# Kernel tuning notes

Measured on AMD Instinct MI355X. Metric: run time of the kernel, lower is better.

Reference implementation:

```python
import jax, jax.numpy as jnp
import numpy as np

CODE_DIM = 512
NUM_CODEBOOKS = 4
CODEBOOK_SIZE = 1024
SUB_DIM = CODE_DIM // NUM_CODEBOOKS


def setup_inputs() -> dict:
    key = jax.random.key(0)
    k1, k2 = jax.random.split(key)
    z_e = jax.random.normal(k1, (64, 512, CODE_DIM), dtype=jnp.float32)
    bound = 1.0 / CODEBOOK_SIZE
    codebooks = jax.random.uniform(
        k2, (NUM_CODEBOOKS, CODEBOOK_SIZE, SUB_DIM),
        minval=-bound, maxval=bound, dtype=jnp.float32)
    return {"z_e": z_e, "codebooks": codebooks}


def reference(z_e, codebooks):
    B, L, D = z_e.shape
    K, S, d = codebooks.shape  # K codebooks, S entries, sub_dim d
    N = B * L
    flat = z_e.reshape(N, K, d)  # per-codebook sub-vectors
    # squared euclidean distances: [N, K, S]
    dist = ((flat ** 2).sum(-1)[:, :, None]
            - 2.0 * jnp.einsum('nkd,ksd->nks', flat, codebooks)
            + (codebooks ** 2).sum(-1)[None, :, :])
    idx = jnp.argmin(dist, axis=-1)  # [N, K]
    # gather nearest codes per codebook
    z_q = codebooks[jnp.arange(K)[None, :], idx]  # [N, K, d]
    z_q_all = z_q.reshape(B, L, D)
    # sum_k mse_k / K == mean over the full concatenated tensor
    codebook_loss = jnp.mean((z_q_all - jax.lax.stop_gradient(z_e)) ** 2)
    commit_loss = jnp.mean((z_e - jax.lax.stop_gradient(z_q_all)) ** 2)
    # perplexity via index counts (no NxS one-hot materialization)
    counts = jnp.zeros((K, S), dtype=z_e.dtype).at[
        jnp.broadcast_to(jnp.arange(K)[None, :], idx.shape), idx].add(1.0)
    avg_probs = counts / N  # [K, S]
    perplexity = jnp.exp(
        -(avg_probs * jnp.log(jnp.clip(avg_probs, 1e-8))).sum(-1)).mean()
    z_q_st = z_e + jax.lax.stop_gradient(z_q_all - z_e)
    indices_all = idx.reshape(B, L, K)
    return indices_all, z_q_st, z_q_all, codebook_loss, commit_loss, perplexity
```

## Files before the change

kernel.cpp:

```cpp
#include <hip/hip_runtime.h>
#include <math.h>

#define NVEC  32768
#define DDIM  512
#define KCB   4
#define SCB   1024
#define SUBD  128

#define IDX_COUNT (NVEC * KCB)
#define ZQ_COUNT  (NVEC * DDIM)
#define OFF_ZQ_ST  IDX_COUNT
#define OFF_ZQ_ALL (IDX_COUNT + ZQ_COUNT)
#define OFF_SCAL   (IDX_COUNT + 2 * ZQ_COUNT)


typedef _Float16 v2h __attribute__((ext_vector_type(2)));
typedef _Float16 f16x8 __attribute__((ext_vector_type(8)));
typedef float f32x16 __attribute__((ext_vector_type(16)));
union U32H2 { unsigned int u; v2h h; };

__device__ __forceinline__ float fmul(float a, float b) { return __fmul_rn(a, b); }
__device__ __forceinline__ float fadd(float a, float b) { return __fadd_rn(a, b); }
__device__ __forceinline__ float fsub(float a, float b) { return __fsub_rn(a, b); }

__device__ __forceinline__ float np_dot128(const float* __restrict__ u,
                                           const float* __restrict__ v) {
  float r[8];
#pragma unroll
  for (int j = 0; j < 8; ++j) r[j] = fmul(u[j], v[j]);
#pragma unroll
  for (int i = 8; i < 128; i += 8) {
#pragma unroll
    for (int j = 0; j < 8; ++j) r[j] = fadd(r[j], fmul(u[i + j], v[i + j]));
  }
  return fadd(fadd(fadd(r[0], r[1]), fadd(r[2], r[3])),
              fadd(fadd(r[4], r[5]), fadd(r[6], r[7])));
}

__device__ __forceinline__ int imin(int a, int b) { return a < b ? a : b; }
__device__ __forceinline__ int imax(int a, int b) { return a > b ? a : b; }

__device__ __forceinline__ void ins4(int& k0, int& k1, int& k2, int& k3, int x) {
  int a = imax(k0, x); k0 = imin(k0, x);
  int b = imax(k1, a); k1 = imin(k1, a);
  int c = imax(k2, b); k2 = imin(k2, b);
  k3 = imin(k3, c);
}

__global__ __launch_bounds__(256) void k_prep(
    const float* __restrict__ cb, unsigned int* __restrict__ cb16,
    float* __restrict__ c2s, float* __restrict__ c2np,
    int* __restrict__ counts, float* __restrict__ scal,
    int* __restrict__ ctrs) {
  const int gt = blockIdx.x * 256 + threadIdx.x;
  if (gt < KCB * SCB) counts[gt] = 0;
  if (gt < 3) scal[gt] = 0.0f;
  if (gt < 2) ctrs[gt] = 0;
  if (gt < KCB * SCB) {
    const float* row = cb + (size_t)gt * SUBD;
    c2np[gt] = np_dot128(row, row);
  }
  const int wave = blockIdx.x * 4 + (threadIdx.x >> 6);
  const int lane = threadIdx.x & 63;
  for (int i = 0; i < 16; ++i) {
    const int code = wave * 16 + i;
    const float2 v = ((const float2*)(cb + (size_t)code * SUBD))[lane];
    float tot = fmaf(v.x, v.x, v.y * v.y);
#pragma unroll
    for (int off = 32; off > 0; off >>= 1) tot += __shfl_down(tot, off, 64);
    v2h h; h.x = (_Float16)(v.x * 1024.0f); h.y = (_Float16)(v.y * 1024.0f);
    U32H2 t; t.h = h;
    cb16[(size_t)code * 64 + lane] = t.u;
    if (lane == 0) c2s[code] = tot * 1048576.0f;
  }
}

#define SCORE(ACC, STOFF, K0, K1, K2, K3)                                    \
  {                                                                          \
    _Pragma("unroll")                                                        \
    for (int g = 0; g < 4; ++g) {                                            \
      const float4 cv = *(const float4*)(c2b + (STOFF) + hi * 4 + g * 8);    \
      const float ca[4] = {cv.x, cv.y, cv.z, cv.w};                          \
      _Pragma("unroll")                                                      \
      for (int r = 0; r < 4; ++r) {                                          \
        const float sc = fmaf(-2048.0f, (ACC)[g * 4 + r], ca[r]);            \
        const int key = ((int)sc << 10) | (tb + (STOFF) + hi * 4 + g * 8 + r); \
        ins4(K0, K1, K2, K3, key);                                           \
      }                                                                      \
    }                                                                        \
  }

__device__ __forceinline__ void stage_tile(const uint4* __restrict__ gsrc,
                                           unsigned int* lds_u32,
                                           int w, int rbase, int ss) {
#pragma unroll
  for (int p = 0; p < 4; ++p) {
    const uint4* src = gsrc + (size_t)((p * 16 + rbase) * 16 + ss);
    unsigned int* dst = lds_u32 + (p * 256 + w * 64) * 4;
    __builtin_amdgcn_global_load_lds(
        (const __attribute__((address_space(1))) unsigned int*)src,
        (__attribute__((address_space(3))) unsigned int*)dst, 16, 0, 0);
  }
}

__global__ __launch_bounds__(256) void k_scan(
    const float* __restrict__ z_e, const unsigned int* __restrict__ cb16,
    const float* __restrict__ c2s, unsigned short* __restrict__ cand) {
  const int tid = threadIdx.x;
  const int lane = tid & 63;
  const int w = tid >> 6;
  const int hi = lane >> 5;
  const int ml = lane & 31;
  const int k = blockIdx.y;
  const int n = blockIdx.x * 128 + w * 32 + ml;

  __shared__ __align__(16) unsigned int ctile[2][4096];

  const uint4* gk = (const uint4*)cb16 + (size_t)k * SCB * 16;
  const float* c2k = c2s + k * SCB;
  const int rbase = tid >> 4;
  const int ss = (tid & 15) ^ rbase;

  f16x8 xf[8];
  {
    const float* xp = z_e + (size_t)n * DDIM + k * SUBD + hi * 8;
#pragma unroll
    for (int ks = 0; ks < 8; ++ks) {
      const float4 a = *(const float4*)(xp + ks * 16);
      const float4 b = *(const float4*)(xp + ks * 16 + 4);
      f16x8 h;
      h[0] = (_Float16)a.x; h[1] = (_Float16)a.y;
      h[2] = (_Float16)a.z; h[3] = (_Float16)a.w;
      h[4] = (_Float16)b.x; h[5] = (_Float16)b.y;
      h[6] = (_Float16)b.z; h[7] = (_Float16)b.w;
      xf[ks] = h;
    }
  }

  stage_tile(gk, ctile[0], w, rbase, ss);
  __syncthreads();

  int kA0 = 0x7FFFFFFF, kA1 = 0x7FFFFFFF, kA2 = 0x7FFFFFFF, kA3 = 0x7FFFFFFF;
  int kB0 = 0x7FFFFFFF, kB1 = 0x7FFFFFFF, kB2 = 0x7FFFFFFF, kB3 = 0x7FFFFFFF;

  for (int tile = 0; tile < 16; ++tile) {
    if (tile < 15)
      stage_tile(gk + (size_t)(tile + 1) * 1024, ctile[(tile + 1) & 1],
                 w, rbase, ss);

    const unsigned char* bufb = (const unsigned char*)ctile[tile & 1];
    f32x16 acc0, acc1;
#pragma unroll
    for (int z = 0; z < 16; ++z) { acc0[z] = 0.0f; acc1[z] = 0.0f; }

#pragma unroll
    for (int ks = 0; ks < 8; ++ks) {
      const int phys = (((ks * 2 + hi) ^ (lane & 15)) << 4);
      const f16x8 a0 = *(const f16x8*)(bufb + ml * 256 + phys);
      const f16x8 a1 = *(const f16x8*)(bufb + (ml + 32) * 256 + phys);
      acc0 = __builtin_amdgcn_mfma_f32_32x32x16_f16(a0, xf[ks], acc0, 0, 0, 0);
      acc1 = __builtin_amdgcn_mfma_f32_32x32x16_f16(a1, xf[ks], acc1, 0, 0, 0);
    }

    const int tb = tile * 64;
    const float* c2b = c2k + tb;
    SCORE(acc0, 0, kA0, kA1, kA2, kA3)
    SCORE(acc1, 32, kB0, kB1, kB2, kB3)

    __syncthreads();
  }

  ins4(kA0, kA1, kA2, kA3, kB0);
  ins4(kA0, kA1, kA2, kA3, kB1);
  ins4(kA0, kA1, kA2, kA3, kB2);
  ins4(kA0, kA1, kA2, kA3, kB3);

  const unsigned long long pk =
      (unsigned long long)(unsigned short)(kA0 & 1023) |
      ((unsigned long long)(unsigned short)(kA1 & 1023) << 16) |
      ((unsigned long long)(unsigned short)(kA2 & 1023) << 32) |
      ((unsigned long long)(unsigned short)(kA3 & 1023) << 48);
  *(unsigned long long*)(cand + ((size_t)(n * KCB + k)) * 8 + hi * 4) = pk;
}

__global__ __launch_bounds__(256) void k_merge(
    const float* __restrict__ z_e, const float* __restrict__ cb,
    const unsigned short* __restrict__ cand, const float* __restrict__ c2np,
    float* __restrict__ out_idx, int* __restrict__ counts,
    float* __restrict__ scal, int* __restrict__ ctrs) {
  const int tid = threadIdx.x;
  const int g = blockIdx.x * 256 + tid;
  const int n = g >> 2, k = g & 3;
  const int w = tid >> 6, lane = tid & 63;

  float4 xv[32];
  const float4* xp = (const float4*)(z_e + (size_t)n * DDIM + k * SUBD);
#pragma unroll
  for (int j = 0; j < 32; ++j) xv[j] = xp[j];
  const float* xs = (const float*)xv;
  const float A = np_dot128(xs, xs);

  const unsigned short* cp = cand + (size_t)g * 8;
  float bd = 1e30f;
  int bi = SCB;
#pragma unroll
  for (int t = 0; t < 8; ++t) {
    const int s = cp[t];
    const float* c = cb + (size_t)(k * SCB + s) * SUBD;
    const float E = np_dot128(xs, c);
    const float dist = fadd(fsub(A, fmul(2.0f, E)), c2np[k * SCB + s]);
    if (dist < bd || (dist == bd && s < bi)) { bd = dist; bi = s; }
  }

  out_idx[g] = (float)bi;
  atomicAdd(&counts[k * SCB + bi], 1);

  float local = bd;
#pragma unroll
  for (int off = 32; off > 0; off >>= 1) local += __shfl_down(local, off, 64);
  __shared__ float red[4];
  if (lane == 0) red[w] = local;
  __syncthreads();

  __shared__ int lastf;
  if (tid == 0) {
    atomicAdd(&scal[0], (red[0] + red[1]) + (red[2] + red[3]));
    __threadfence();
    lastf = (atomicAdd(&ctrs[0], 1) == (int)gridDim.x - 1);
  }
  __syncthreads();

  if (lastf) {
    double h = 0.0;
    for (int i = 0; i < SCB / 64; ++i) {
      const int cnt = __hip_atomic_load(&counts[w * SCB + i * 64 + lane],
                                        __ATOMIC_RELAXED, __HIP_MEMORY_SCOPE_AGENT);
      if (cnt > 0) {
        const double p = (double)cnt * (1.0 / 32768.0);
        h += p * log(p);
      }
    }
#pragma unroll
    for (int off = 32; off > 0; off >>= 1) h += __shfl_down(h, off, 64);
    __shared__ double hs[4];
    if (lane == 0) hs[w] = h;
    __syncthreads();
    if (tid == 0) {
      double perp = 0.0;
      for (int w2 = 0; w2 < 4; ++w2) perp += exp(-hs[w2]);
      scal[2] = (float)(perp * 0.25);
      const float L = __hip_atomic_load(&scal[0], __ATOMIC_RELAXED,
                                        __HIP_MEMORY_SCOPE_AGENT);
      const float m = L * (1.0f / 16777216.0f);
      scal[0] = m;
      scal[1] = m;
    }
  }
}

__global__ __launch_bounds__(256) void k_gather(
    const float* __restrict__ cb, const float* __restrict__ idxf,
    float* __restrict__ zq_st, float* __restrict__ zq_all) {
  const int base = blockIdx.x * 4096;
#pragma unroll
  for (int i = 0; i < 16; ++i) {
    const int q = base + i * 256 + threadIdx.x;
    const int nn = q >> 7;
    const int rem = q & 127;
    const int kk = rem >> 5;
    const int j4 = rem & 31;
    const int idx = (int)idxf[nn * KCB + kk];
    const float4 v = ((const float4*)cb)[(size_t)(kk * SCB + idx) * 32 + j4];
    ((float4*)zq_st)[q] = v;
    ((float4*)zq_all)[q] = v;
  }
}

extern "C" void kernel_launch(void* const* d_in, const int* in_sizes, int n_in,
                              void* d_out, int out_size, void* d_ws, size_t ws_size,
                              hipStream_t stream) {
  const float* z_e = (const float*)d_in[0];
  const float* cb = (const float*)d_in[1];
  float* out = (float*)d_out;

  float* zq_all = out + OFF_ZQ_ALL;
  int* counts = (int*)zq_all;
  float* c2s = zq_all + 4096;
  float* c2np = zq_all + 8192;
  unsigned int* cb16 = (unsigned int*)(zq_all + 12288);
  unsigned short* cand = (unsigned short*)(zq_all + 274432);
  int* ctrs = (int*)(zq_all + 800000);
  float* scal = out + OFF_SCAL;

  k_prep<<<64, 256, 0, stream>>>(cb, cb16, c2s, c2np, counts, scal, ctrs);
  dim3 gs(NVEC / 128, KCB);
  k_scan<<<gs, 256, 0, stream>>>(z_e, cb16, c2s, cand);
  k_merge<<<IDX_COUNT / 256, 256, 0, stream>>>(z_e, cb, cand, c2np, out, counts,
                                               scal, ctrs);
  k_gather<<<1024, 256, 0, stream>>>(cb, out, out + OFF_ZQ_ST, zq_all);
}
```

Baseline: 351.6 us.

## Spread merge candidate distance evaluation across lanes with shuffle argmin

```diff
diff --git a/kernel.cpp b/kernel.cpp
--- a/kernel.cpp
+++ b/kernel.cpp
@@ -189,33 +189,41 @@
     float* __restrict__ out_idx, int* __restrict__ counts,
     float* __restrict__ scal, int* __restrict__ ctrs) {
   const int tid = threadIdx.x;
-  const int g = blockIdx.x * 256 + tid;
-  const int n = g >> 2, k = g & 3;
   const int w = tid >> 6, lane = tid & 63;
-
-  float4 xv[32];
-  const float4* xp = (const float4*)(z_e + (size_t)n * DDIM + k * SUBD);
-#pragma unroll
-  for (int j = 0; j < 32; ++j) xv[j] = xp[j];
-  const float* xs = (const float*)xv;
-  const float A = np_dot128(xs, xs);
-
-  const unsigned short* cp = cand + (size_t)g * 8;
+  const int n = blockIdx.x * 4 + w;
+  const int k = (lane & 31) >> 3;
+  const int c = lane & 7;
+  const int isE = (lane < 32);
+
+  const int g = n * KCB + k;
+  const int s = cand[(size_t)g * 8 + c];
+
+  const float* xrow = z_e + (size_t)n * DDIM + k * SUBD;
+  const float* vrow = isE ? (cb + (size_t)(k * SCB + s) * SUBD) : xrow;
+
+  const float dot = np_dot128(xrow, vrow);
+  const float Av = __shfl(dot, lane | 32, 64);
+
   float bd = 1e30f;
   int bi = SCB;
-#pragma unroll
-  for (int t = 0; t < 8; ++t) {
-    const int s = cp[t];
-    const float* c = cb + (size_t)(k * SCB + s) * SUBD;
-    const float E = np_dot128(xs, c);
-    const float dist = fadd(fsub(A, fmul(2.0f, E)), c2np[k * SCB + s]);
-    if (dist < bd || (dist == bd && s < bi)) { bd = dist; bi = s; }
-  }
-
-  out_idx[g] = (float)bi;
-  atomicAdd(&counts[k * SCB + bi], 1);
-
-  float local = bd;
+  if (isE) {
+    bd = fadd(fsub(Av, fmul(2.0f, dot)), c2np[k * SCB + s]);
+    bi = s;
+  }
+#pragma unroll
+  for (int off = 1; off <= 4; off <<= 1) {
+    const float od = __shfl_xor(bd, off, 64);
+    const int oi = __shfl_xor(bi, off, 64);
+    if (od < bd || (od == bd && oi < bi)) { bd = od; bi = oi; }
+  }
+
+  const int writer = isE && (c == 0);
+  if (writer) {
+    out_idx[g] = (float)bi;
+    atomicAdd(&counts[k * SCB + bi], 1);
+  }
+
+  float local = writer ? bd : 0.0f;
 #pragma unroll
   for (int off = 32; off > 0; off >>= 1) local += __shfl_down(local, off, 64);
   __shared__ float red[4];
@@ -295,7 +303,7 @@
   k_prep<<<64, 256, 0, stream>>>(cb, cb16, c2s, c2np, counts, scal, ctrs);
   dim3 gs(NVEC / 128, KCB);
   k_scan<<<gs, 256, 0, stream>>>(z_e, cb16, c2s, cand);
-  k_merge<<<IDX_COUNT / 256, 256, 0, stream>>>(z_e, cb, cand, c2np, out, counts,
-                                               scal, ctrs);
+  k_merge<<<NVEC / 4, 256, 0, stream>>>(z_e, cb, cand, c2np, out, counts,
+                                        scal, ctrs);
   k_gather<<<1024, 256, 0, stream>>>(cb, out, out + OFF_ZQ_ST, zq_all);
 }
```

After: 565.3 us. +60.8%, slower.
